# Optimization experiments

Measured on AMD Instinct MI355X. Metric: run time of the kernel, lower is better.

Reference implementation:

```python
import jax, jax.numpy as jnp
import numpy as np

# ---- config constants (from configs) ----
B, L, C = 32, 512, 16
DM, DS, DCONV, EXP, EL = 128, 16, 4, 2, 2
PATCH, STRIDE, PAD, PRED = 16, 8, 8, 96
DIN = EXP * DM            # 256
DTR = (DM + 15) // 16     # dt_rank = 8
NPATCH = (L + 2 * PAD - PATCH) // STRIDE + 1   # 65
HNF = DM * NPATCH         # 8320
EPS = 1e-5


def setup_inputs() -> dict:
    key = jax.random.key(0)
    ks = jax.random.split(key, 14)
    n = jax.random.normal
    A_log = jnp.tile(jnp.log(jnp.arange(1, DS + 1, dtype=jnp.float32)), (EL, DIN, 1))
    return {
        "x_enc": n(ks[0], (B, L, C), jnp.float32),
        "x_mark_enc": n(ks[1], (B, L, 4), jnp.float32),
        "pe_w": n(ks[2], (DM, 1, PATCH), jnp.float32) * (1.0 / np.sqrt(PATCH)),
        "pe_b": n(ks[3], (DM,), jnp.float32) * 0.02,
        "in_proj_w": n(ks[4], (EL, 2 * DIN, DM), jnp.float32) * (1.0 / np.sqrt(DM)),
        "conv_w": n(ks[5], (EL, DIN, DCONV), jnp.float32) * (1.0 / np.sqrt(DCONV)),
        "conv_b": n(ks[6], (EL, DIN), jnp.float32) * 0.02,
        "x_proj_w": n(ks[7], (EL, DTR + 2 * DS, DIN), jnp.float32) * (1.0 / np.sqrt(DIN)),
        "dt_proj_w": n(ks[8], (EL, DIN, DTR), jnp.float32) * (1.0 / np.sqrt(DTR)),
        "dt_proj_b": n(ks[9], (EL, DIN), jnp.float32) * 0.1,
        "A_log": A_log,
        "D": jnp.ones((EL, DIN), jnp.float32),
        "out_proj_w": n(ks[10], (EL, DM, DIN), jnp.float32) * (1.0 / np.sqrt(DIN)),
        "head_w": n(ks[11], (PRED, HNF), jnp.float32) * (1.0 / np.sqrt(HNF)),
    }


def _silu(x):
    return x * jax.nn.sigmoid(x)


def _mamba(x, in_w, cw, cb, xp_w, dtp_w, dtp_b, A_log, Dp, out_w):
    # x: (b, P, DM)
    b = x.shape[0]
    xz = jnp.einsum('bpd,ed->bpe', x, in_w)            # (b, P, 2*DIN)
    xin, z = jnp.split(xz, 2, axis=-1)
    # causal depthwise conv1d over time
    xt = xin.transpose(0, 2, 1)                        # (b, DIN, P)
    conv = jax.lax.conv_general_dilated(
        xt, cw[:, None, :], (1,), [(DCONV - 1, 0)],
        dimension_numbers=('NCH', 'OIH', 'NCH'), feature_group_count=DIN)
    xc = _silu((conv + cb[None, :, None]).transpose(0, 2, 1))   # (b, P, DIN)
    dbc = jnp.einsum('bpd,ed->bpe', xc, xp_w)          # (b, P, DTR+2*DS)
    dt, Bm, Cm = jnp.split(dbc, [DTR, DTR + DS], axis=-1)
    dt = jax.nn.softplus(jnp.einsum('bpr,dr->bpd', dt, dtp_w) + dtp_b)  # (b,P,DIN)
    A = -jnp.exp(A_log)                                # (DIN, DS)

    def step(h, inp):
        dt_t, B_t, C_t, x_t = inp                      # (b,DIN),(b,DS),(b,DS),(b,DIN)
        dA = jnp.exp(dt_t[:, :, None] * A)             # (b,DIN,DS)
        h = dA * h + (dt_t * x_t)[:, :, None] * B_t[:, None, :]
        y = jnp.einsum('bds,bs->bd', h, C_t)
        return h, y

    h0 = jnp.zeros((b, DIN, DS), x.dtype)
    xs = (dt.transpose(1, 0, 2), Bm.transpose(1, 0, 2),
          Cm.transpose(1, 0, 2), xc.transpose(1, 0, 2))
    _, ys = jax.lax.scan(step, h0, xs)                 # (P, b, DIN)
    y = ys.transpose(1, 0, 2) + xc * Dp
    y = y * _silu(z)
    return jnp.einsum('bpd,od->bpo', y, out_w)         # (b, P, DM)


def reference(x_enc, x_mark_enc, pe_w, pe_b, in_proj_w, conv_w, conv_b,
              x_proj_w, dt_proj_w, dt_proj_b, A_log, D, out_proj_w, head_w):
    # RevIN-style normalization (stats detached, as in torch)
    mean = jax.lax.stop_gradient(jnp.mean(x_enc, axis=1, keepdims=True))
    xc = x_enc - mean
    std = jax.lax.stop_gradient(jnp.sqrt(jnp.var(xc, axis=1, keepdims=True) + EPS))
    xn = xc / std                                      # (B, L, C)
    x = xn.transpose(0, 2, 1).reshape(B * C, 1, L)
    # patch embedding conv
    p = jax.lax.conv_general_dilated(
        x, pe_w, (STRIDE,), [(PAD, PAD)],
        dimension_numbers=('NCH', 'OIH', 'NCH')) + pe_b[None, :, None]
    p = p.transpose(0, 2, 1)                           # (B*C, NPATCH, DM)
    for i in range(EL):
        p = _mamba(p, in_proj_w[i], conv_w[i], conv_b[i], x_proj_w[i],
                   dt_proj_w[i], dt_proj_b[i], A_log[i], D[i], out_proj_w[i])
    flat = p.reshape(B * C, HNF)
    head = flat @ head_w.T                             # (B*C, PRED)
    out = head.reshape(B, C, PRED).transpose(0, 2, 1)  # (B, PRED, C)
    return out * std + mean
```

## Files before the change

### kernel.cpp

```cpp
#include <hip/hip_runtime.h>

typedef __attribute__((ext_vector_type(8))) short bf16x8;
typedef __attribute__((ext_vector_type(8))) unsigned short u16x8;
typedef __attribute__((ext_vector_type(4))) float f32x4;

#define DEV static __device__ __forceinline__

constexpr int DM   = 128;
constexpr int DIN  = 256;
constexpr int NP   = 65;
constexpr int NSEQ = 512;
constexpr int HNF  = 8320;
constexpr int LOPL = NSEQ*HNF;

constexpr size_t OFF_FLAG = 0;
constexpr size_t OFF_MEAN = 16;
constexpr size_t OFF_STD  = OFF_MEAN + 512;
constexpr size_t OFF_ANEG = OFF_STD  + 512;
constexpr size_t OFF_CONVW= OFF_ANEG + 8192;
constexpr size_t OFF_CONVB= OFF_CONVW+ 2048;
constexpr size_t OFF_DTPB = OFF_CONVB+ 512;
constexpr size_t OFF_DD   = OFF_DTPB + 512;
constexpr size_t OFF_PEWT = OFF_DD   + 512;
constexpr size_t OFF_PEB  = OFF_PEWT + 2048;
constexpr size_t OFF_INF  = OFF_PEB  + 128;
constexpr size_t OFF_XPF  = OFF_INF  + 65536;
constexpr size_t OFF_OPF  = OFF_XPF  + 12288;
constexpr size_t OFF_HDF  = OFF_OPF  + 32768;
constexpr size_t OFF_PA   = OFF_HDF  + 399360;
constexpr size_t OFF_PB   = OFF_PA   + (size_t)NSEQ*HNF;
constexpr size_t OFF_HACC = OFF_PB;

DEV float b2f(unsigned short u){ union{unsigned v; float f;} x; x.v = ((unsigned)u)<<16; return x.f; }
DEV unsigned short f2b(float f){
  union{float f32; unsigned u;} x; x.f32 = f;
  unsigned r = x.u + 0x7fffu + ((x.u>>16)&1u);
  return (unsigned short)(r>>16);
}
DEV void split2(float v, unsigned short& h, unsigned short& l){
  h = f2b(v); l = f2b(v - b2f(h));
}
DEV float load_in(const void* p, size_t i, int isbf){
  return isbf ? b2f(((const unsigned short*)p)[i]) : ((const float*)p)[i];
}
DEV f32x4 mfma16(bf16x8 a, bf16x8 b, f32x4 c){
  return __builtin_amdgcn_mfma_f32_16x16x32_bf16(a,b,c,0,0,0);
}
constexpr float LOG2E = 1.4426950408889634f;
constexpr float LN2   = 0.6931471805599453f;
DEV float ex2(float x){ float r; asm("v_exp_f32 %0, %1" : "=v"(r) : "v"(x)); return r; }
DEV float lg2(float x){ float r; asm("v_log_f32 %0, %1" : "=v"(r) : "v"(x)); return r; }
DEV float frcp(float x){ float r; asm("v_rcp_f32 %0, %1" : "=v"(r) : "v"(x)); return r; }
DEV float sigm(float x){ return frcp(1.f + ex2(-x*LOG2E)); }
DEV float softplus(float x){
  float t = ex2(-fabsf(x)*LOG2E);
  return fmaxf(x,0.f) + LN2*lg2(1.f + t);
}
DEV int detect_bf16_wave(const void* x, int tid){
  const unsigned short* u = (const unsigned short*)x;
  unsigned short v = u[2*tid];
  int e = (v>>7)&0xff;
  int pred = (v==0) || (e>=100 && e<=141);
  unsigned long long m = __ballot(pred);
  return __popcll(m) >= 48;
}
DEV u16x8 load8_cvt(const void* p, size_t off, int isbf){
  u16x8 o;
  if (isbf){
    o = *(const u16x8*)((const unsigned short*)p + off);
  } else {
    const float* s = (const float*)p + off;
    float4 a = *(const float4*)(s), b = *(const float4*)(s+4);
    o[0]=f2b(a.x); o[1]=f2b(a.y); o[2]=f2b(a.z); o[3]=f2b(a.w);
    o[4]=f2b(b.x); o[5]=f2b(b.y); o[6]=f2b(b.z); o[7]=f2b(b.w);
  }
  return o;
}

constexpr size_t N_SMALL = 13952;
constexpr size_t N_IN8 = 16384, N_XP8 = 3072, N_OP8 = 8192, N_HD8 = 99840;
constexpr size_t N_BIG8 = N_IN8+N_XP8+N_OP8+N_HD8;
constexpr int NPREP = (int)((N_SMALL + N_BIG8 + 255)/256);
__global__ void k_pre(const void* x_enc, const void* pe_w, const void* pe_b,
                      const void* in_w, const void* conv_w, const void* conv_b,
                      const void* xp_w, const void* dtp_b,
                      const void* A_log, const void* Dm, const void* op_w,
                      const void* head_w, float* __restrict__ ws)
{
  const int tid = threadIdx.x;
  __shared__ int sflag;
  __shared__ float sx[512];
  __shared__ float spe[16*128];
  __shared__ float spb[128];
  __shared__ float rs[8], rq[8], sm[2];

  if (tid < 64){
    int f = detect_bf16_wave(x_enc, tid);
    if (tid==0) sflag = f;
  }
  __syncthreads();
  const int isbf = sflag;

  if (blockIdx.x < NPREP){
    if (blockIdx.x==0 && tid==0) ws[OFF_FLAG] = (float)isbf;
    size_t i = (size_t)blockIdx.x*256 + tid;
    const size_t nA=8192, nCW=2048, nCB=512, nDB=512, nD=512, nPW=2048, nPB=128;
    if (i < N_SMALL){
      if (i < nA){ ws[OFF_ANEG+i] = -__expf(load_in(A_log,i,isbf)); return; } i -= nA;
      if (i < nCW){ ws[OFF_CONVW+i] = load_in(conv_w,i,isbf); return; } i -= nCW;
      if (i < nCB){ ws[OFF_CONVB+i] = load_in(conv_b,i,isbf); return; } i -= nCB;
      if (i < nDB){ ws[OFF_DTPB+i]  = load_in(dtp_b,i,isbf); return; } i -= nDB;
      if (i < nD){  ws[OFF_DD+i]    = load_in(Dm,i,isbf); return; } i -= nD;
      if (i < nPW){ size_t k=i>>7, dm=i&127; ws[OFF_PEWT+i]=load_in(pe_w, dm*16+k, isbf); return; } i -= nPW;
      ws[OFF_PEB+i] = load_in(pe_b,i,isbf); return;
    }
    size_t i8 = i - N_SMALL;
    if (i8 >= N_BIG8) return;
    if (i8 < N_IN8){
      size_t lane=i8&63, kk=(i8>>6)&3, nt=(i8>>8)&31, l=i8>>13;
      size_t e=nt*16+(lane&15), k0=kk*32+((lane>>4)*8);
      ((u16x8*)((unsigned short*)(ws+OFF_INF)))[i8] =
        load8_cvt(in_w, (l*512+e)*128 + k0, isbf);
      return;
    } i8 -= N_IN8;
    if (i8 < N_XP8){
      size_t lane=i8&63, kk=(i8>>6)&7; size_t rest=i8>>9;
      size_t nt=rest%3, l=rest/3;
      size_t o=nt*16+(lane&15), k0=kk*32+((lane>>4)*8);
      u16x8 v;
      if (o<40) v = load8_cvt(xp_w, (l*40+o)*256 + k0, isbf);
      else { u16x8 z = {0,0,0,0,0,0,0,0}; v = z; }
      ((u16x8*)((unsigned short*)(ws+OFF_XPF)))[i8] = v;
      return;
    } i8 -= N_XP8;
    if (i8 < N_OP8){
      size_t lane=i8&63, kk=(i8>>6)&7, nt=(i8>>9)&7, l=i8>>12;
      size_t dm=nt*16+(lane&15), k0=kk*32+((lane>>4)*8);
      ((u16x8*)((unsigned short*)(ws+OFF_OPF)))[i8] =
        load8_cvt(op_w, (l*128+dm)*256 + k0, isbf);
      return;
    } i8 -= N_OP8;
    {
      size_t lane=i8&63, t=i8>>6;
      size_t kk=t%260, nt=t/260;
      size_t pr=nt*16+(lane&15), k0=kk*32+((lane>>4)*8);
      ((u16x8*)((unsigned short*)(ws+OFF_HDF)))[i8] =
        load8_cvt(head_w, pr*8320 + k0, isbf);
      return;
    }
  }

  const int n = blockIdx.x - NPREP;
  const int b = n>>4, c = n&15;

  float v0 = load_in(x_enc, ((size_t)b*512+tid)*16 + c, isbf);
  float v1 = load_in(x_enc, ((size_t)b*512+tid+256)*16 + c, isbf);
  float s = v0+v1, q = v0*v0+v1*v1;
  for (int o=32;o;o>>=1){ s += __shfl_down(s,o,64); q += __shfl_down(q,o,64); }
  const int w = tid>>6, lane = tid&63;
  if (lane==0){ rs[w]=s; rq[w]=q; }
  __syncthreads();
  if (tid==0){
    float S=rs[0]+rs[1]+rs[2]+rs[3], Q=rq[0]+rq[1]+rq[2]+rq[3];
    float mean = S*(1.f/512.f);
    float var = fmaxf(Q*(1.f/512.f)-mean*mean, 0.f);
    float sd = sqrtf(var+1e-5f);
    sm[0]=mean; sm[1]=1.f/sd;
    ws[OFF_MEAN+n]=mean; ws[OFF_STD+n]=sd;
  }
  __syncthreads();
  const float mean=sm[0], rstd=sm[1];
  sx[tid]=(v0-mean)*rstd; sx[tid+256]=(v1-mean)*rstd;
  for (int i=tid;i<2048;i+=256) spe[i]=load_in(pe_w, (size_t)(i&127)*16 + (i>>7), isbf);
  if (tid<128) spb[tid]=load_in(pe_b, tid, isbf);
  __syncthreads();

  unsigned short* pa_hi = (unsigned short*)(ws+OFF_PA);
  unsigned short* pa_lo = pa_hi + LOPL;
  for (int i=tid;i<NP*DM;i+=256){
    int t=i>>7, dm=i&127;
    float acc = spb[dm];
    int j0 = t*8-8;
    #pragma unroll
    for (int k=0;k<16;k++){ int j=j0+k; if ((unsigned)j<512u) acc += sx[j]*spe[k*128+dm]; }
    unsigned short h,lo2; split2(acc,h,lo2);
    pa_hi[(size_t)n*HNF+i] = h;
    pa_lo[(size_t)n*HNF+i] = lo2;
  }
}

__global__ __launch_bounds__(256,2)
void k_layer(int l, const unsigned short* __restrict__ pin,
             unsigned short* __restrict__ pout, float* __restrict__ ws,
             const void* __restrict__ dtp_w_raw)
{
  const int n = blockIdx.x, tid = threadIdx.x;
  const int w = tid>>6, lane = tid&63, ml = lane&15, quad = lane>>4;
  const int isbf = ws[OFF_FLAG] != 0.f;

  __shared__ __align__(16) unsigned char arena[79040];
  unsigned short* s_hi = (unsigned short*)arena;
  unsigned short* s_lo = (unsigned short*)(arena+34320);
  float* s_dbc = (float*)(arena+68640);

  const unsigned short* INF = (const unsigned short*)(ws+OFF_INF) + (size_t)l*65536;
  const unsigned short* XPF = (const unsigned short*)(ws+OFF_XPF) + (size_t)l*12288;
  const unsigned short* OPF = (const unsigned short*)(ws+OFF_OPF) + (size_t)l*32768;
  const unsigned short* phi = pin + (size_t)n*HNF;
  const unsigned short* plo = phi + LOPL;

  for (int pass=0; pass<2; ++pass){
    f32x4 acc[5][2];
    #pragma unroll
    for (int mt=0;mt<5;mt++){
      #pragma unroll
      for (int p2=0;p2<2;p2++){ f32x4 z={0.f,0.f,0.f,0.f}; acc[mt][p2]=z; }
    }
    bf16x8 ah[2][5], al[2][5];
    #pragma unroll
    for (int mt=0;mt<5;mt++){
      int row = mt*16+ml; if (row>64) row=64;
      ah[0][mt] = *(const bf16x8*)&phi[(size_t)row*128 + quad*8];
      al[0][mt] = *(const bf16x8*)&plo[(size_t)row*128 + quad*8];
    }
    #pragma unroll
    for (int kk=0;kk<4;kk++){
      const int cur = kk&1, nxt = cur^1;
      bf16x8 b0 = *(const bf16x8*)&INF[((size_t)((pass*8+w*2+0)*4+kk))*512 + lane*8];
      bf16x8 b1 = *(const bf16x8*)&INF[((size_t)((pass*8+w*2+1)*4+kk))*512 + lane*8];
      if (kk<3){
        #pragma unroll
        for (int mt=0;mt<5;mt++){
          int row = mt*16+ml; if (row>64) row=64;
          ah[nxt][mt] = *(const bf16x8*)&phi[(size_t)row*128 + (kk+1)*32 + quad*8];
          al[nxt][mt] = *(const bf16x8*)&plo[(size_t)row*128 + (kk+1)*32 + quad*8];
        }
      }
      #pragma unroll
      for (int mt=0;mt<5;mt++)
        acc[mt][0] = mfma16(ah[cur][mt],b0,mfma16(al[cur][mt],b0,acc[mt][0]));
      #pragma unroll
      for (int mt=0;mt<5;mt++)
        acc[mt][1] = mfma16(ah[cur][mt],b1,mfma16(al[cur][mt],b1,acc[mt][1]));
    }
    #pragma unroll
    for (int p2=0;p2<2;p2++){
      int e = (pass*8 + w*2 + p2)*16 + ml;
      #pragma unroll
      for (int mt=0;mt<5;mt++){
        #pragma unroll
        for (int r=0;r<4;r++){
          int t = mt*16+quad*4+r;
          if (t<NP){
            unsigned short h,lo2; split2(acc[mt][p2][r],h,lo2);
            s_hi[t*264+e]=h; s_lo[t*264+e]=lo2;
          }
        }
      }
    }
  }
  __syncthreads();

  {
    const int d = tid;
    const float4 wv = ((const float4*)(ws+OFF_CONVW))[l*256+d];
    const float bb = ws[OFF_CONVB + l*256+d];
    float x0=0.f,x1=0.f,x2=0.f;
    int t = 0;
    for (; t+4<=NP; t+=4){
      float xi0 = b2f(s_hi[(t+0)*264+d]) + b2f(s_lo[(t+0)*264+d]);
      float xi1 = b2f(s_hi[(t+1)*264+d]) + b2f(s_lo[(t+1)*264+d]);
      float xi2 = b2f(s_hi[(t+2)*264+d]) + b2f(s_lo[(t+2)*264+d]);
      float xi3 = b2f(s_hi[(t+3)*264+d]) + b2f(s_lo[(t+3)*264+d]);
      float v0 = bb + wv.x*x0  + wv.y*x1  + wv.z*x2  + wv.w*xi0;
      float v1 = bb + wv.x*x1  + wv.y*x2  + wv.z*xi0 + wv.w*xi1;
      float v2 = bb + wv.x*x2  + wv.y*xi0 + wv.z*xi1 + wv.w*xi2;
      float v3 = bb + wv.x*xi0 + wv.y*xi1 + wv.z*xi2 + wv.w*xi3;
      x0=xi1; x1=xi2; x2=xi3;
      float s0 = v0*sigm(v0), s1 = v1*sigm(v1), s2 = v2*sigm(v2), s3 = v3*sigm(v3);
      unsigned short h,lo2;
      split2(s0,h,lo2); s_hi[(t+0)*264+d]=h; s_lo[(t+0)*264+d]=lo2;
      split2(s1,h,lo2); s_hi[(t+1)*264+d]=h; s_lo[(t+1)*264+d]=lo2;
      split2(s2,h,lo2); s_hi[(t+2)*264+d]=h; s_lo[(t+2)*264+d]=lo2;
      split2(s3,h,lo2); s_hi[(t+3)*264+d]=h; s_lo[(t+3)*264+d]=lo2;
    }
    for (; t<NP; ++t){
      float xi = b2f(s_hi[t*264+d]) + b2f(s_lo[t*264+d]);
      float v = bb + wv.x*x0 + wv.y*x1 + wv.z*x2 + wv.w*xi;
      x0=x1; x1=x2; x2=xi;
      float sv = v * sigm(v);
      unsigned short h,lo2; split2(sv,h,lo2);
      s_hi[t*264+d]=h; s_lo[t*264+d]=lo2;
    }
  }
  __syncthreads();

  for (int tile=w; tile<15; tile+=4){
    int mt=tile/3, nt=tile%3;
    f32x4 acc={0.f,0.f,0.f,0.f};
    #pragma unroll
    for (int kk=0;kk<8;kk++){
      int row = mt*16+ml; if (row>64) row=64;
      bf16x8 ah = *(const bf16x8*)&s_hi[row*264 + kk*32 + quad*8];
      bf16x8 al = *(const bf16x8*)&s_lo[row*264 + kk*32 + quad*8];
      bf16x8 b  = *(const bf16x8*)&XPF[((size_t)(nt*8+kk))*512 + lane*8];
      acc = mfma16(ah,b,mfma16(al,b,acc));
    }
    int o = nt*16+ml;
    #pragma unroll
    for (int r=0;r<4;r++){
      int t=mt*16+quad*4+r;
      if (t<NP && o<40) s_dbc[t*40+o] = acc[r];
    }
  }
  __syncthreads();

  {
    const int d = tid;
    float A2[16];
    {
      const float4* ap = (const float4*)(ws+OFF_ANEG) + ((size_t)l*256+d)*4;
      #pragma unroll
      for (int qq=0;qq<4;qq++){
        float4 t4 = ap[qq];
        A2[qq*4]=t4.x*LOG2E; A2[qq*4+1]=t4.y*LOG2E; A2[qq*4+2]=t4.z*LOG2E; A2[qq*4+3]=t4.w*LOG2E;
      }
    }
    int fastbit = 1;
    #pragma unroll
    for (int ss=0;ss<16;ss++){
      float ex = -(float)(ss+1)*LOG2E;
      fastbit &= (fabsf(A2[ss]-ex) <= 1e-4f*(float)(ss+1)) ? 1 : 0;
    }
    const int fastu = __all(fastbit);
    const float Dv = ws[OFF_DD + l*256+d];
    const float bias = ws[OFF_DTPB + l*256+d];
    float wdt[8];
    #pragma unroll
    for (int r=0;r<8;r++) wdt[r] = load_in(dtp_w_raw, ((size_t)l*256+d)*8+r, isbf);
    float h[16];
    #pragma unroll
    for (int ss=0;ss<16;ss++) h[ss]=0.f;

    float4 q0 = *(const float4*)&s_dbc[0];
    float4 q1 = *(const float4*)&s_dbc[4];
    float xh = b2f(s_hi[d]), xl = b2f(s_lo[d]);

    for (int t=0;t<NP;t++){
      const float* row = &s_dbc[t*40];
      float xv = xh + xl;
      float4 b0=*(const float4*)(row+8),  b1=*(const float4*)(row+12),
             b2v=*(const float4*)(row+16), b3=*(const float4*)(row+20);
      float4 c0=*(const float4*)(row+24), c1=*(const float4*)(row+28),
             c2=*(const float4*)(row+32), c3=*(const float4*)(row+36);
      float4 nq0, nq1; float nxh=0.f, nxl=0.f;
      if (t+1<NP){
        const float* nrow = &s_dbc[(t+1)*40];
        nq0 = *(const float4*)(nrow);
        nq1 = *(const float4*)(nrow+4);
        nxh = b2f(s_hi[(t+1)*264+d]); nxl = b2f(s_lo[(t+1)*264+d]);
      }
      float p0 = q0.x*wdt[0] + q0.y*wdt[1];
      float p1 = q0.z*wdt[2] + q0.w*wdt[3];
      float p2 = q1.x*wdt[4] + q1.y*wdt[5];
      float p3 = q1.z*wdt[6] + q1.w*wdt[7];
      float din = (bias + p0 + p1) + (p2 + p3);
      float dtv = softplus(din);
      float dtx = dtv*xv;
      float Bv[16], Cv[16];
      Bv[0]=b0.x;Bv[1]=b0.y;Bv[2]=b0.z;Bv[3]=b0.w; Bv[4]=b1.x;Bv[5]=b1.y;Bv[6]=b1.z;Bv[7]=b1.w;
      Bv[8]=b2v.x;Bv[9]=b2v.y;Bv[10]=b2v.z;Bv[11]=b2v.w; Bv[12]=b3.x;Bv[13]=b3.y;Bv[14]=b3.z;Bv[15]=b3.w;
      Cv[0]=c0.x;Cv[1]=c0.y;Cv[2]=c0.z;Cv[3]=c0.w; Cv[4]=c1.x;Cv[5]=c1.y;Cv[6]=c1.z;Cv[7]=c1.w;
      Cv[8]=c2.x;Cv[9]=c2.y;Cv[10]=c2.z;Cv[11]=c2.w; Cv[12]=c3.x;Cv[13]=c3.y;Cv[14]=c3.z;Cv[15]=c3.w;
      float rr[16];
      if (fastu){
        float r1 = ex2(-dtv*LOG2E);
        float r2=r1*r1;
        float r3=r2*r1, r4=r2*r2;
        float r5=r4*r1, r6=r4*r2, r7=r4*r3, r8=r4*r4;
        rr[0]=r1; rr[1]=r2; rr[2]=r3; rr[3]=r4;
        rr[4]=r5; rr[5]=r6; rr[6]=r7; rr[7]=r8;
        rr[8]=r8*r1; rr[9]=r8*r2; rr[10]=r8*r3; rr[11]=r8*r4;
        rr[12]=r8*r5; rr[13]=r8*r6; rr[14]=r8*r7; rr[15]=r8*r8;
      } else {
        #pragma unroll
        for (int ss=0;ss<16;ss++) rr[ss] = ex2(dtv*A2[ss]);
      }
      float y0 = 0.f, y1 = 0.f;
      #pragma unroll
      for (int ss=0;ss<16;ss+=2){
        h[ss]   = rr[ss]*h[ss]     + dtx*Bv[ss];
        h[ss+1] = rr[ss+1]*h[ss+1] + dtx*Bv[ss+1];
        y0 += h[ss]*Cv[ss];
        y1 += h[ss+1]*Cv[ss+1];
      }
      float g0 = (y0+y1) + xv*Dv;
      unsigned short hh,lo2; split2(g0,hh,lo2);
      s_hi[t*264+d]=hh; s_lo[t*264+d]=lo2;
      q0=nq0; q1=nq1; xh=nxh; xl=nxl;
    }
  }
  __syncthreads();

  {
    bf16x8 ah[2][4], al[2][4];
    {
      int row = ml;
      #pragma unroll
      for (int kk=0;kk<4;kk++){
        ah[0][kk] = *(const bf16x8*)&phi[(size_t)row*128 + kk*32 + quad*8];
        al[0][kk] = *(const bf16x8*)&plo[(size_t)row*128 + kk*32 + quad*8];
      }
    }
    #pragma unroll
    for (int mt=0; mt<5; ++mt){
      const int cur = mt&1, nxt = cur^1;
      if (mt<4){
        int row = (mt+1)*16+ml; if (row>64) row=64;
        #pragma unroll
        for (int kk=0;kk<4;kk++){
          ah[nxt][kk] = *(const bf16x8*)&phi[(size_t)row*128 + kk*32 + quad*8];
          al[nxt][kk] = *(const bf16x8*)&plo[(size_t)row*128 + kk*32 + quad*8];
        }
      }
      #pragma unroll
      for (int j=0;j<4;j++){
        int nt = w + j*4;
        f32x4 acc={0.f,0.f,0.f,0.f};
        #pragma unroll
        for (int kk=0;kk<4;kk++){
          bf16x8 b = *(const bf16x8*)&INF[((size_t)((16+nt)*4+kk))*512 + lane*8];
          acc = mfma16(ah[cur][kk],b,mfma16(al[cur][kk],b,acc));
        }
        int d = nt*16+ml;
        #pragma unroll
        for (int r=0;r<4;r++){
          int t = mt*16+quad*4+r;
          if (t<NP){
            float g0 = b2f(s_hi[t*264+d]) + b2f(s_lo[t*264+d]);
            float zv = acc[r];
            float g = g0 * zv * sigm(zv);
            unsigned short hh,lo2; split2(g,hh,lo2);
            s_hi[t*264+d]=hh; s_lo[t*264+d]=lo2;
          }
        }
      }
    }
  }
  __syncthreads();

  {
    f32x4 acc[5][2];
    #pragma unroll
    for (int mt=0;mt<5;mt++){
      #pragma unroll
      for (int p2=0;p2<2;p2++){ f32x4 z={0.f,0.f,0.f,0.f}; acc[mt][p2]=z; }
    }
    bf16x8 bpre[2][2];
    bpre[0][0] = *(const bf16x8*)&OPF[((size_t)((w*2+0)*8+0))*512 + lane*8];
    bpre[0][1] = *(const bf16x8*)&OPF[((size_t)((w*2+1)*8+0))*512 + lane*8];
    #pragma unroll
    for (int kk=0;kk<8;kk++){
      const int cur = kk&1, nxt = cur^1;
      if (kk<7){
        bpre[nxt][0] = *(const bf16x8*)&OPF[((size_t)((w*2+0)*8+kk+1))*512 + lane*8];
        bpre[nxt][1] = *(const bf16x8*)&OPF[((size_t)((w*2+1)*8+kk+1))*512 + lane*8];
      }
      bf16x8 ah[5], al[5];
      #pragma unroll
      for (int mt=0;mt<5;mt++){
        int row = mt*16+ml; if (row>64) row=64;
        ah[mt] = *(const bf16x8*)&s_hi[row*264 + kk*32 + quad*8];
        al[mt] = *(const bf16x8*)&s_lo[row*264 + kk*32 + quad*8];
      }
      #pragma unroll
      for (int mt=0;mt<5;mt++)
        acc[mt][0] = mfma16(ah[mt],bpre[cur][0],mfma16(al[mt],bpre[cur][0],acc[mt][0]));
      #pragma unroll
      for (int mt=0;mt<5;mt++)
        acc[mt][1] = mfma16(ah[mt],bpre[cur][1],mfma16(al[mt],bpre[cur][1],acc[mt][1]));
    }
    #pragma unroll
    for (int p2=0;p2<2;p2++){
      int dm = (w*2+p2)*16+ml;
      #pragma unroll
      for (int mt=0;mt<5;mt++){
        #pragma unroll
        for (int r=0;r<4;r++){
          int t = mt*16+quad*4+r;
          if (t<NP){
            unsigned short hh,lo2; split2(acc[mt][p2][r],hh,lo2);
            pout[(size_t)n*HNF + t*128 + dm] = hh;
            pout[(size_t)n*HNF + t*128 + dm + LOPL] = lo2;
          }
        }
      }
    }
  }
}

__global__ void k_headp(const float* __restrict__ ws, float* __restrict__ hacc)
{
  const int blk = blockIdx.x;
  const int p = blk & 3, tile = blk >> 2;
  const int nt = tile%6, mt = tile/6;
  const int tid = threadIdx.x, w = tid>>6, lane = tid&63, ml = lane&15, quad = lane>>4;
  const unsigned short* pa_hi = (const unsigned short*)(ws+OFF_PA);
  const unsigned short* pa_lo = pa_hi + LOPL;
  const unsigned short* HDF = (const unsigned short*)(ws+OFF_HDF);
  __shared__ float red[4][64][4];

  f32x4 acc={0.f,0.f,0.f,0.f};
  const size_t abase = (size_t)(mt*16+ml)*HNF + quad*8;
  for (int i=w; i<65; i+=4){
    int kk = p*65 + i;
    bf16x8 ah = *(const bf16x8*)(pa_hi + abase + (size_t)kk*32);
    bf16x8 al = *(const bf16x8*)(pa_lo + abase + (size_t)kk*32);
    bf16x8 b = *(const bf16x8*)&HDF[((size_t)(nt*260+kk))*512 + lane*8];
    acc = mfma16(ah,b,mfma16(al,b,acc));
  }
  #pragma unroll
  for (int r=0;r<4;r++) red[w][lane][r]=acc[r];
  __syncthreads();
  if (w==0){
    #pragma unroll
    for (int r=0;r<4;r++){
      float s = red[0][lane][r]+red[1][lane][r]+red[2][lane][r]+red[3][lane][r];
      hacc[((size_t)tile*4 + p)*256 + lane*4 + r] = s;
    }
  }
}

__global__ void k_fin(const float* __restrict__ ws, void* __restrict__ out)
{
  const int tile = blockIdx.x;
  const int nt = tile%6, mt = tile/6;
  const int lane = threadIdx.x, ml = lane&15, quad = lane>>4;
  const float* hacc = ws + OFF_HACC;
  const int isbf = ws[OFF_FLAG]!=0.f;
  #pragma unroll
  for (int r=0;r<4;r++){
    size_t base = (size_t)tile*4*256 + lane*4 + r;
    float s = hacc[base] + hacc[base+256] + hacc[base+512] + hacc[base+768];
    int nseq = mt*16 + quad*4 + r;
    int pred = nt*16 + ml;
    float val = s*ws[OFF_STD+nseq] + ws[OFF_MEAN+nseq];
    size_t o = ((size_t)(nseq>>4)*96 + pred)*16 + (nseq&15);
    if (isbf) ((unsigned short*)out)[o] = f2b(val);
    else      ((float*)out)[o] = val;
  }
}

extern "C" void kernel_launch(void* const* d_in, const int* in_sizes, int n_in,
                              void* d_out, int out_size, void* d_ws, size_t ws_size,
                              hipStream_t stream)
{
  (void)in_sizes; (void)n_in; (void)out_size; (void)ws_size;
  float* ws = (float*)d_ws;
  const void* x_enc = d_in[0];
  const void* pe_w  = d_in[2];  const void* pe_b  = d_in[3];
  const void* in_w  = d_in[4];  const void* conv_w= d_in[5];
  const void* conv_b= d_in[6];  const void* xp_w  = d_in[7];
  const void* dtp_w = d_in[8];  const void* dtp_b = d_in[9];
  const void* A_log = d_in[10]; const void* Dm    = d_in[11];
  const void* op_w  = d_in[12]; const void* head_w= d_in[13];

  k_pre<<<NPREP+NSEQ,256,0,stream>>>(x_enc,pe_w,pe_b,in_w,conv_w,conv_b,xp_w,
                                     dtp_b,A_log,Dm,op_w,head_w,ws);
  unsigned short* pa = (unsigned short*)(ws+OFF_PA);
  unsigned short* pb = (unsigned short*)(ws+OFF_PB);
  k_layer<<<NSEQ,256,0,stream>>>(0,pa,pb,ws,dtp_w);
  k_layer<<<NSEQ,256,0,stream>>>(1,pb,pa,ws,dtp_w);
  k_headp<<<768,256,0,stream>>>(ws, ws+OFF_HACC);
  k_fin<<<192,64,0,stream>>>(ws, d_out);
}
```

Measured before the change: 266.0 us.

## Read head weights directly in head GEMM and fuse finalize via atomic counter

Drops the pre-pass that repacked head_w into an MFMA-friendly bf16 layout and instead loads and converts head_w rows directly inside k_headp. It also removes the separate k_fin launch: each tile's four split-K blocks bump an atomic counter, and the last one sums the partials and writes the denormalized output. This saves one kernel launch plus a large weight-copy pass, at the cost of uncoalesced strided head_w loads and a counter that is reset in the prep kernel.

```diff
diff --git a/kernel.cpp b/kernel.cpp
--- a/kernel.cpp
+++ b/kernel.cpp
@@ -76,16 +76,17 @@
   }
   return o;
 }
+DEV bf16x8 as_bf(u16x8 v){ union{u16x8 u; bf16x8 b;} x; x.u=v; return x.b; }
 
 constexpr size_t N_SMALL = 13952;
-constexpr size_t N_IN8 = 16384, N_XP8 = 3072, N_OP8 = 8192, N_HD8 = 99840;
-constexpr size_t N_BIG8 = N_IN8+N_XP8+N_OP8+N_HD8;
+constexpr size_t N_IN8 = 16384, N_XP8 = 3072, N_OP8 = 8192;
+constexpr size_t N_BIG8 = N_IN8+N_XP8+N_OP8;
 constexpr int NPREP = (int)((N_SMALL + N_BIG8 + 255)/256);
 __global__ void k_pre(const void* x_enc, const void* pe_w, const void* pe_b,
                       const void* in_w, const void* conv_w, const void* conv_b,
                       const void* xp_w, const void* dtp_b,
                       const void* A_log, const void* Dm, const void* op_w,
-                      const void* head_w, float* __restrict__ ws)
+                      float* __restrict__ ws)
 {
   const int tid = threadIdx.x;
   __shared__ int sflag;
@@ -102,7 +103,10 @@
   const int isbf = sflag;
 
   if (blockIdx.x < NPREP){
-    if (blockIdx.x==0 && tid==0) ws[OFF_FLAG] = (float)isbf;
+    if (blockIdx.x==0){
+      if (tid==0) ws[OFF_FLAG] = (float)isbf;
+      if (tid<192) ((unsigned*)(ws+OFF_HDF))[tid] = 0u;
+    }
     size_t i = (size_t)blockIdx.x*256 + tid;
     const size_t nA=8192, nCW=2048, nCB=512, nDB=512, nD=512, nPW=2048, nPB=128;
     if (i < N_SMALL){
@@ -133,19 +137,11 @@
       ((u16x8*)((unsigned short*)(ws+OFF_XPF)))[i8] = v;
       return;
     } i8 -= N_XP8;
-    if (i8 < N_OP8){
+    {
       size_t lane=i8&63, kk=(i8>>6)&7, nt=(i8>>9)&7, l=i8>>12;
       size_t dm=nt*16+(lane&15), k0=kk*32+((lane>>4)*8);
       ((u16x8*)((unsigned short*)(ws+OFF_OPF)))[i8] =
         load8_cvt(op_w, (l*128+dm)*256 + k0, isbf);
-      return;
-    } i8 -= N_OP8;
-    {
-      size_t lane=i8&63, t=i8>>6;
-      size_t kk=t%260, nt=t/260;
-      size_t pr=nt*16+(lane&15), k0=kk*32+((lane>>4)*8);
-      ((u16x8*)((unsigned short*)(ws+OFF_HDF)))[i8] =
-        load8_cvt(head_w, pr*8320 + k0, isbf);
       return;
     }
   }
@@ -499,24 +495,29 @@
   }
 }
 
-__global__ void k_headp(const float* __restrict__ ws, float* __restrict__ hacc)
+__global__ void k_headp(float* __restrict__ ws, const void* __restrict__ head_w,
+                        void* __restrict__ out)
 {
   const int blk = blockIdx.x;
   const int p = blk & 3, tile = blk >> 2;
   const int nt = tile%6, mt = tile/6;
   const int tid = threadIdx.x, w = tid>>6, lane = tid&63, ml = lane&15, quad = lane>>4;
+  const int isbf = ws[OFF_FLAG]!=0.f;
   const unsigned short* pa_hi = (const unsigned short*)(ws+OFF_PA);
   const unsigned short* pa_lo = pa_hi + LOPL;
-  const unsigned short* HDF = (const unsigned short*)(ws+OFF_HDF);
+  float* hacc = ws + OFF_HACC;
+  unsigned* cnt = (unsigned*)(ws + OFF_HDF);
   __shared__ float red[4][64][4];
+  __shared__ unsigned slast;
 
   f32x4 acc={0.f,0.f,0.f,0.f};
   const size_t abase = (size_t)(mt*16+ml)*HNF + quad*8;
+  const size_t brow  = (size_t)(nt*16+ml)*8320 + quad*8;
   for (int i=w; i<65; i+=4){
     int kk = p*65 + i;
     bf16x8 ah = *(const bf16x8*)(pa_hi + abase + (size_t)kk*32);
     bf16x8 al = *(const bf16x8*)(pa_lo + abase + (size_t)kk*32);
-    bf16x8 b = *(const bf16x8*)&HDF[((size_t)(nt*260+kk))*512 + lane*8];
+    bf16x8 b  = as_bf(load8_cvt(head_w, brow + (size_t)kk*32, isbf));
     acc = mfma16(ah,b,mfma16(al,b,acc));
   }
   #pragma unroll
@@ -529,25 +530,25 @@
       hacc[((size_t)tile*4 + p)*256 + lane*4 + r] = s;
     }
   }
-}
-
-__global__ void k_fin(const float* __restrict__ ws, void* __restrict__ out)
-{
-  const int tile = blockIdx.x;
-  const int nt = tile%6, mt = tile/6;
-  const int lane = threadIdx.x, ml = lane&15, quad = lane>>4;
-  const float* hacc = ws + OFF_HACC;
-  const int isbf = ws[OFF_FLAG]!=0.f;
-  #pragma unroll
-  for (int r=0;r<4;r++){
-    size_t base = (size_t)tile*4*256 + lane*4 + r;
-    float s = hacc[base] + hacc[base+256] + hacc[base+512] + hacc[base+768];
-    int nseq = mt*16 + quad*4 + r;
-    int pred = nt*16 + ml;
-    float val = s*ws[OFF_STD+nseq] + ws[OFF_MEAN+nseq];
-    size_t o = ((size_t)(nseq>>4)*96 + pred)*16 + (nseq&15);
-    if (isbf) ((unsigned short*)out)[o] = f2b(val);
-    else      ((float*)out)[o] = val;
+  __threadfence();
+  __syncthreads();
+  if (tid==0) slast = atomicAdd(&cnt[tile], 1u);
+  __syncthreads();
+  if (slast==3u){
+    __threadfence();
+    if (w==0){
+      #pragma unroll
+      for (int r=0;r<4;r++){
+        size_t base = (size_t)tile*4*256 + lane*4 + r;
+        float s = hacc[base] + hacc[base+256] + hacc[base+512] + hacc[base+768];
+        int nseq = mt*16 + quad*4 + r;
+        int pred = nt*16 + ml;
+        float val = s*ws[OFF_STD+nseq] + ws[OFF_MEAN+nseq];
+        size_t o = ((size_t)(nseq>>4)*96 + pred)*16 + (nseq&15);
+        if (isbf) ((unsigned short*)out)[o] = f2b(val);
+        else      ((float*)out)[o] = val;
+      }
+    }
   }
 }
 
@@ -566,11 +567,10 @@
   const void* op_w  = d_in[12]; const void* head_w= d_in[13];
 
   k_pre<<<NPREP+NSEQ,256,0,stream>>>(x_enc,pe_w,pe_b,in_w,conv_w,conv_b,xp_w,
-                                     dtp_b,A_log,Dm,op_w,head_w,ws);
+                                     dtp_b,A_log,Dm,op_w,ws);
   unsigned short* pa = (unsigned short*)(ws+OFF_PA);
   unsigned short* pb = (unsigned short*)(ws+OFF_PB);
   k_layer<<<NSEQ,256,0,stream>>>(0,pa,pb,ws,dtp_w);
   k_layer<<<NSEQ,256,0,stream>>>(1,pb,pa,ws,dtp_w);
-  k_headp<<<768,256,0,stream>>>(ws, ws+OFF_HACC);
-  k_fin<<<192,64,0,stream>>>(ws, d_out);
-}
+  k_headp<<<768,256,0,stream>>>(ws, head_w, d_out);
+}
```

New measurement: 343.3 us. 29.0% more time.

## Reuse head activation loads across all six output tiles per block

Applied to the files above, without the earlier changes.

Restructures the head GEMM split-K kernel so that each block covers all six prediction tiles for one row tile, loading the A fragments (hi/lo) once and reusing them across six MFMA accumulators. K is split into eight chunks with 512-thread blocks, and the final reduction sums eight partials instead of four. This cuts redundant activation reads from global memory, but adds register pressure and more serialized LDS reductions.

```diff
diff --git a/kernel.cpp b/kernel.cpp
--- a/kernel.cpp
+++ b/kernel.cpp
@@ -499,35 +499,48 @@
   }
 }
 
-__global__ void k_headp(const float* __restrict__ ws, float* __restrict__ hacc)
+__global__ __launch_bounds__(512,2)
+void k_headp(const float* __restrict__ ws, float* __restrict__ hacc)
 {
   const int blk = blockIdx.x;
-  const int p = blk & 3, tile = blk >> 2;
-  const int nt = tile%6, mt = tile/6;
+  const int p = blk & 7, mt = blk >> 3;
   const int tid = threadIdx.x, w = tid>>6, lane = tid&63, ml = lane&15, quad = lane>>4;
+  const int base  = (p<4) ? p*33 : 132 + (p-4)*32;
+  const int count = (p<4) ? 33 : 32;
   const unsigned short* pa_hi = (const unsigned short*)(ws+OFF_PA);
   const unsigned short* pa_lo = pa_hi + LOPL;
   const unsigned short* HDF = (const unsigned short*)(ws+OFF_HDF);
-  __shared__ float red[4][64][4];
-
-  f32x4 acc={0.f,0.f,0.f,0.f};
+  __shared__ float red[8][64][4];
+
+  f32x4 acc[6];
+  #pragma unroll
+  for (int nt=0;nt<6;nt++){ f32x4 z={0.f,0.f,0.f,0.f}; acc[nt]=z; }
+
   const size_t abase = (size_t)(mt*16+ml)*HNF + quad*8;
-  for (int i=w; i<65; i+=4){
-    int kk = p*65 + i;
+  for (int i=w; i<count; i+=8){
+    const int kk = base + i;
     bf16x8 ah = *(const bf16x8*)(pa_hi + abase + (size_t)kk*32);
     bf16x8 al = *(const bf16x8*)(pa_lo + abase + (size_t)kk*32);
-    bf16x8 b = *(const bf16x8*)&HDF[((size_t)(nt*260+kk))*512 + lane*8];
-    acc = mfma16(ah,b,mfma16(al,b,acc));
-  }
-  #pragma unroll
-  for (int r=0;r<4;r++) red[w][lane][r]=acc[r];
-  __syncthreads();
-  if (w==0){
-    #pragma unroll
-    for (int r=0;r<4;r++){
-      float s = red[0][lane][r]+red[1][lane][r]+red[2][lane][r]+red[3][lane][r];
-      hacc[((size_t)tile*4 + p)*256 + lane*4 + r] = s;
-    }
+    #pragma unroll
+    for (int nt=0;nt<6;nt++){
+      bf16x8 b = *(const bf16x8*)&HDF[((size_t)(nt*260+kk))*512 + lane*8];
+      acc[nt] = mfma16(ah,b,mfma16(al,b,acc[nt]));
+    }
+  }
+
+  for (int nt=0;nt<6;nt++){
+    #pragma unroll
+    for (int r=0;r<4;r++) red[w][lane][r] = acc[nt][r];
+    __syncthreads();
+    if (w==0){
+      #pragma unroll
+      for (int r=0;r<4;r++){
+        float s = red[0][lane][r]+red[1][lane][r]+red[2][lane][r]+red[3][lane][r]
+                + red[4][lane][r]+red[5][lane][r]+red[6][lane][r]+red[7][lane][r];
+        hacc[((size_t)(mt*6+nt)*8 + p)*256 + lane*4 + r] = s;
+      }
+    }
+    __syncthreads();
   }
 }
 
@@ -540,8 +553,10 @@
   const int isbf = ws[OFF_FLAG]!=0.f;
   #pragma unroll
   for (int r=0;r<4;r++){
-    size_t base = (size_t)tile*4*256 + lane*4 + r;
-    float s = hacc[base] + hacc[base+256] + hacc[base+512] + hacc[base+768];
+    size_t base = (size_t)tile*8*256 + lane*4 + r;
+    float s = 0.f;
+    #pragma unroll
+    for (int p=0;p<8;p++) s += hacc[base + (size_t)p*256];
     int nseq = mt*16 + quad*4 + r;
     int pred = nt*16 + ml;
     float val = s*ws[OFF_STD+nseq] + ws[OFF_MEAN+nseq];
@@ -571,6 +586,6 @@
   unsigned short* pb = (unsigned short*)(ws+OFF_PB);
   k_layer<<<NSEQ,256,0,stream>>>(0,pa,pb,ws,dtp_w);
   k_layer<<<NSEQ,256,0,stream>>>(1,pb,pa,ws,dtp_w);
-  k_headp<<<768,256,0,stream>>>(ws, ws+OFF_HACC);
+  k_headp<<<256,512,0,stream>>>(ws, ws+OFF_HACC);
   k_fin<<<192,64,0,stream>>>(ws, d_out);
 }
```

Measured after the change: 254.3 us (median of 2 runs). 1.05x faster.
